# Kernel optimization log

Measured on AMD Instinct MI355X. Metric: run time of the kernel, lower is better.

The kernel has to match this reference:

```python
import jax, jax.numpy as jnp
import numpy as np

VOXEL_SIZE = 0.4
STRIDE = 2
NUM_BATCH = 4
PRE_MAXSIZE = 1024  # nms_premaxsize
NMS_THR = 0.1
NEG_INF = -1e9


def setup_inputs() -> dict:
    key = jax.random.key(0)
    ks = jax.random.split(key, 7)
    N, C = 200000, 256
    feat = jax.random.normal(ks[0], (N, C), dtype=jnp.float32)
    batch_idx = jax.random.randint(ks[1], (N,), 0, NUM_BATCH, dtype=jnp.int32)
    coor = jax.random.randint(ks[2], (N, 2), 0, 400, dtype=jnp.int32)
    W_cls = jax.random.normal(ks[3], (C, 2), dtype=jnp.float32) * 0.02
    b_cls = jnp.zeros((2,), dtype=jnp.float32)
    W_reg = jax.random.normal(ks[4], (C, 9), dtype=jnp.float32) * 0.02
    b_reg = jnp.zeros((9,), dtype=jnp.float32)
    return {"feat": feat, "batch_idx": batch_idx, "coor": coor,
            "W_cls": W_cls, "b_cls": b_cls, "W_reg": W_reg, "b_reg": b_reg}


def _bev_iou(bx):
    # bx: [K,7] (x,y,z,l,w,h,r); axis-aligned BEV IoU on (x,y,l,w)
    x, y, l, w = bx[:, 0], bx[:, 1], bx[:, 3], bx[:, 4]
    x1, x2 = x - l / 2, x + l / 2
    y1, y2 = y - w / 2, y + w / 2
    ix = jnp.maximum(jnp.minimum(x2[:, None], x2[None, :]) - jnp.maximum(x1[:, None], x1[None, :]), 0.0)
    iy = jnp.maximum(jnp.minimum(y2[:, None], y2[None, :]) - jnp.maximum(y1[:, None], y1[None, :]), 0.0)
    inter = ix * iy
    area = l * w
    union = area[:, None] + area[None, :] - inter
    return inter / jnp.maximum(union, 1e-6)


def _nms_keep(iou):
    # greedy NMS over score-descending rows; returns keep mask [K]
    K = iou.shape[0]
    idx = jnp.arange(K)

    def body(i, supp):
        keep_i = jnp.logical_not(supp[i])
        new = keep_i & (iou[i] > NMS_THR) & (idx > i)
        return supp | new

    supp = jax.lax.fori_loop(0, K, body, jnp.zeros((K,), dtype=bool))
    return jnp.logical_not(supp)


def reference(feat, batch_idx, coor, W_cls, b_cls, W_reg, b_reg):
    # ---- shared heads over all sparse voxels ----
    cls_logits = feat @ W_cls + b_cls            # [N, 1+1] (neg evidence, class)
    probs = jax.nn.softmax(cls_logits, axis=-1)
    cls_prob = probs[:, 1:]                      # [N, n_cls]
    conf = jnp.max(cls_prob, axis=-1)            # [N]
    label = jnp.argmax(cls_prob, axis=-1)        # [N]

    reg = feat @ W_reg + b_reg                   # [N, 9] -> ctr(3) dim(3) dir(2) scr(1)
    ctr, dim, drn, scr = reg[:, :3], reg[:, 3:6], reg[:, 6:8], reg[:, 8]
    scr = jax.nn.sigmoid(scr)                    # sigmoid_keys=['scr']

    # indices2metric: voxel indices -> metric centers
    centers = coor.astype(jnp.float32) * (VOXEL_SIZE * STRIDE)  # [N, 2]

    xy = centers + ctr[:, :2]
    z = ctr[:, 2]
    lwh = jnp.exp(jnp.clip(dim, -6.0, 6.0))
    angle = jnp.arctan2(drn[:, 0], drn[:, 1])
    boxes = jnp.concatenate([xy, z[:, None], lwh, angle[:, None]], axis=-1)  # [N, 7]
    score = conf * scr                           # [N]

    def per_sample(b):
        s = jnp.where(batch_idx == b, score, NEG_INF)
        vals, idx = jax.lax.top_k(s, PRE_MAXSIZE)          # score-sorted (desc)
        bx = boxes[idx]                                     # [K, 7]
        lb = label[idx]                                     # [K]
        valid = vals > NEG_INF / 2
        iou = _bev_iou(bx)
        keep = _nms_keep(iou) & valid
        out = jnp.concatenate([bx, vals[:, None]], axis=-1) * keep[:, None]  # [K, 8]
        return out, lb, keep

    out, lb, keep = jax.vmap(per_sample)(jnp.arange(NUM_BATCH))
    return out, lb, keep
```

## Files before the change

### kernel.cpp

```cpp
#include <hip/hip_runtime.h>
#include <math.h>

#define NBATCH 4
#define PRE 1024
#define CAND 4096
#define NHIST 65536
#define MAXSLOT 384

__device__ __forceinline__ unsigned long long allow_mask(int i, int l) {
    int base = l << 6;
    if (i < base) return ~0ull;
    int sh = i - base + 1;
    if (sh >= 64) return 0ull;
    return (~0ull) << sh;
}

__global__ void k0_weights(const float* __restrict__ Wcls, const float* __restrict__ bcls,
                           const float* __restrict__ Wreg, const float* __restrict__ breg,
                           double* __restrict__ Wd3, float* __restrict__ Wf8,
                           double* __restrict__ biasD, float* __restrict__ biasF) {
    int j = blockIdx.x;
    int c = threadIdx.x;
    if (j < 2) {
        Wd3[j * 256 + c] = (double)Wcls[c * 2 + j];
        if (c == 0) biasD[j] = (double)bcls[j];
    } else if (j == 10) {
        Wd3[2 * 256 + c] = (double)Wreg[c * 9 + 8];
        if (c == 0) biasD[2] = (double)breg[8];
    } else {
        int r = j - 2;
        Wf8[r * 256 + c] = Wreg[c * 9 + r];
        if (c == 0) biasF[r] = breg[r];
    }
}

__global__ __launch_bounds__(256) void k1_points(
    const float4* __restrict__ feat4, const int* __restrict__ batch_idx,
    const int* __restrict__ coor, const double* __restrict__ Wd3,
    const float* __restrict__ Wf8, const double* __restrict__ biasD,
    const float* __restrict__ biasF, float* __restrict__ pointData,
    unsigned long long* __restrict__ keys, unsigned int* __restrict__ hist, int N) {
    __shared__ float4 smem4[64 * 68 / 4];
    float* sfeat = (float*)smem4;
    int tid = threadIdx.x;
    int q = tid >> 6;
    int p = tid & 63;
    int p0 = blockIdx.x * 64;

    double accD0 = 0.0, accD1 = 0.0, accD2 = 0.0;
    float accF[8];
#pragma unroll
    for (int j = 0; j < 8; ++j) accF[j] = 0.f;

    for (int c = 0; c < 4; ++c) {
        __syncthreads();
#pragma unroll
        for (int it = 0; it < 4; ++it) {
            int u = it * 256 + tid;
            int pl = u >> 4, f4 = u & 15;
            int gp = p0 + pl;
            float4 v = make_float4(0.f, 0.f, 0.f, 0.f);
            if (gp < N) v = feat4[(size_t)gp * 64 + c * 16 + f4];
            *(float4*)(sfeat + pl * 68 + f4 * 4) = v;
        }
        __syncthreads();
        int chb = c * 64 + q * 16;
        const double* w0 = Wd3 + chb;
        const float* wf = Wf8 + chb;
#pragma unroll
        for (int k4 = 0; k4 < 4; ++k4) {
            float4 v = *(const float4*)(sfeat + p * 68 + q * 16 + k4 * 4);
            float vv[4] = {v.x, v.y, v.z, v.w};
#pragma unroll
            for (int m = 0; m < 4; ++m) {
                int k = k4 * 4 + m;
                double fd = (double)vv[m];
                accD0 = fma(fd, w0[k], accD0);
                accD1 = fma(fd, w0[256 + k], accD1);
                accD2 = fma(fd, w0[512 + k], accD2);
#pragma unroll
                for (int j = 0; j < 8; ++j) accF[j] = fmaf(vv[m], wf[j * 256 + k], accF[j]);
            }
        }
    }
    __syncthreads();
    double* pD = (double*)smem4;
    float* pF = (float*)smem4 + 1536;
    pD[tid * 3 + 0] = accD0; pD[tid * 3 + 1] = accD1; pD[tid * 3 + 2] = accD2;
#pragma unroll
    for (int j = 0; j < 8; ++j) pF[tid * 8 + j] = accF[j];
    __syncthreads();
    if (tid < 64) {
        int gp = p0 + tid;
        if (gp < N) {
            double d0 = biasD[0], d1 = biasD[1], d2 = biasD[2];
            float f[8];
#pragma unroll
            for (int j = 0; j < 8; ++j) f[j] = biasF[j];
#pragma unroll
            for (int qq = 0; qq < 4; ++qq) {
                int base = qq * 64 + tid;
                d0 += pD[base * 3 + 0]; d1 += pD[base * 3 + 1]; d2 += pD[base * 3 + 2];
#pragma unroll
                for (int j = 0; j < 8; ++j) f[j] += pF[base * 8 + j];
            }
            double conf = 1.0 / (1.0 + exp(-(d1 - d0)));
            double scr = 1.0 / (1.0 + exp(-d2));
            double score = conf * scr;
            float s32 = (float)score;

            float cx = (float)coor[2 * gp] * 0.8f;
            float cy = (float)coor[2 * gp + 1] * 0.8f;
            float bx = cx + f[0], by = cy + f[1], bz = f[2];
            float bl = expf(fminf(fmaxf(f[3], -6.f), 6.f));
            float bw = expf(fminf(fmaxf(f[4], -6.f), 6.f));
            float bh = expf(fminf(fmaxf(f[5], -6.f), 6.f));
            float ba = atan2f(f[6], f[7]);

            float4* pd = (float4*)(pointData + (size_t)gp * 8);
            pd[0] = make_float4(bx, by, bz, bl);
            pd[1] = make_float4(bw, bh, ba, s32);
            keys[gp] = (unsigned long long)__double_as_longlong(score);
            int b = batch_idx[gp];
            atomicAdd(&hist[b * NHIST + (__float_as_uint(s32) >> 16)], 1u);
        }
    }
}

__global__ __launch_bounds__(256) void k2_thresh(const unsigned int* __restrict__ hist,
                                                 unsigned int* __restrict__ Tarr) {
    int b = blockIdx.x, tid = threadIdx.x;
    __shared__ unsigned int csum[256];
    __shared__ unsigned int chunkv[256];
    __shared__ int stc;
    __shared__ unsigned int scum;
    const unsigned int* h = hist + b * NHIST;
    unsigned int s = 0;
    for (int m = 0; m < 256; ++m) s += h[tid * 256 + m];
    csum[tid] = s;
    __syncthreads();
    if (tid == 0) {
        unsigned int cum = 0; int tc = -1;
        for (int t = 255; t >= 0; --t) {
            if (cum + csum[t] >= 1024u) { tc = t; break; }
            cum += csum[t];
        }
        stc = tc; scum = cum;
    }
    __syncthreads();
    int tc = stc;
    if (tc < 0) { if (tid == 0) Tarr[b] = 0u; return; }
    chunkv[tid] = h[tc * 256 + tid];
    __syncthreads();
    if (tid == 0) {
        unsigned int cum = scum, T = (unsigned int)(tc * 256);
        for (int m = 255; m >= 0; --m) {
            unsigned int c = chunkv[m];
            if (cum + c >= 1024u) { T = (unsigned int)(tc * 256 + m); break; }
            cum += c;
        }
        Tarr[b] = T;
    }
}

__global__ void k3_compact(const int* __restrict__ batch_idx, const float* __restrict__ pointData,
                           const unsigned long long* __restrict__ keys,
                           const unsigned int* __restrict__ Tarr, unsigned int* __restrict__ candCount,
                           unsigned int* __restrict__ candIdx, unsigned long long* __restrict__ candKey,
                           int N) {
    int p = blockIdx.x * 256 + threadIdx.x;
    if (p >= N) return;
    int b = batch_idx[p];
    float s32 = pointData[(size_t)p * 8 + 7];
    unsigned int bucket = __float_as_uint(s32) >> 16;
    if (bucket >= Tarr[b]) {
        unsigned int pos = atomicAdd(&candCount[b], 1u);
        if (pos < CAND) {
            candIdx[b * CAND + pos] = (unsigned int)p;
            candKey[b * CAND + pos] = keys[p];
        }
    }
}

__global__ __launch_bounds__(1024) void k4_sort(const unsigned int* __restrict__ candCount,
                                                const unsigned int* __restrict__ candIdx,
                                                const unsigned long long* __restrict__ candKey,
                                                const float* __restrict__ pointData,
                                                float* __restrict__ topBox,
                                                unsigned int* __restrict__ validArr) {
    int b = blockIdx.x, tid = threadIdx.x;
    __shared__ unsigned long long ka[CAND];
    __shared__ unsigned int id[CAND];
    unsigned int cnt = candCount[b];
    if (cnt > CAND) cnt = CAND;
    int n = (cnt <= 2048u) ? 2048 : 4096;
    for (int t = tid; t < n; t += 1024) {
        if ((unsigned int)t < cnt) {
            ka[t] = ~candKey[b * CAND + t];
            id[t] = candIdx[b * CAND + t];
        } else {
            ka[t] = ~0ull;
            id[t] = 0xFFFFFFFFu;
        }
    }
    __syncthreads();
    for (int k = 2; k <= n; k <<= 1) {
        for (int j = k >> 1; j > 0; j >>= 1) {
            for (int t = tid; t < n; t += 1024) {
                int l = t ^ j;
                if (l > t) {
                    bool up = ((t & k) == 0);
                    unsigned long long kt = ka[t], kl = ka[l];
                    unsigned int it_ = id[t], il = id[l];
                    bool gt = (kt > kl) || (kt == kl && it_ > il);
                    if (gt == up) { ka[t] = kl; ka[l] = kt; id[t] = il; id[l] = it_; }
                }
            }
            __syncthreads();
        }
    }
    unsigned int gi = id[tid];
    bool valid = (gi != 0xFFFFFFFFu) && ((unsigned int)tid < cnt);
    float v[8];
#pragma unroll
    for (int k = 0; k < 8; ++k) v[k] = 0.f;
    if (valid) {
        const float* pd = pointData + (size_t)gi * 8;
#pragma unroll
        for (int k = 0; k < 8; ++k) v[k] = pd[k];
    }
    float* tb = topBox + (size_t)(b * PRE + tid) * 8;
#pragma unroll
    for (int k = 0; k < 8; ++k) tb[k] = v[k];
    validArr[b * PRE + tid] = valid ? 1u : 0u;
}

__global__ __launch_bounds__(256) void k5_iou(const float* __restrict__ topBox,
                                              unsigned long long* __restrict__ M) {
    int wid = blockIdx.x * 4 + (threadIdx.x >> 6);
    int lane = threadIdx.x & 63;
    int b = wid >> 14;
    int rem = wid & 16383;
    int i = rem >> 4;
    int wj = rem & 15;
    if (wj < (i >> 6)) return;
    const float* bi = topBox + (size_t)(b * PRE + i) * 8;
    int j = wj * 64 + lane;
    const float* bj = topBox + (size_t)(b * PRE + j) * 8;
    float xi = bi[0], yi = bi[1], li = bi[3], wi_ = bi[4];
    float xj = bj[0], yj = bj[1], lj = bj[3], wj_ = bj[4];
    float x1i = xi - li * 0.5f, x2i = xi + li * 0.5f;
    float y1i = yi - wi_ * 0.5f, y2i = yi + wi_ * 0.5f;
    float x1j = xj - lj * 0.5f, x2j = xj + lj * 0.5f;
    float y1j = yj - wj_ * 0.5f, y2j = yj + wj_ * 0.5f;
    float ix = fmaxf(fminf(x2i, x2j) - fmaxf(x1i, x1j), 0.0f);
    float iy = fmaxf(fminf(y2i, y2j) - fmaxf(y1i, y1j), 0.0f);
    float inter = ix * iy;
    float ai = li * wi_, aj = lj * wj_;
    float uni = ai + aj - inter;
    float iou = inter / fmaxf(uni, 1e-6f);
    unsigned long long m = __ballot(iou > 0.1f);
    if (lane == 0) M[(size_t)(b * PRE + i) * 16 + wj] = m;
}

__global__ __launch_bounds__(256) void k6_nms(const unsigned long long* __restrict__ M,
                                              const unsigned int* __restrict__ validArr,
                                              const float* __restrict__ topBox,
                                              float* __restrict__ out0,
                                              float* __restrict__ keepOut) {
    __shared__ unsigned long long Mc[MAXSLOT * 16];
    __shared__ unsigned int slotIdx[PRE];
    __shared__ unsigned int cntSh;
    __shared__ unsigned long long suppSh[16];
    int b = blockIdx.x, tid = threadIdx.x;
    if (tid == 0) cntSh = 0;
    __syncthreads();
    for (int r = tid; r < PRE; r += 256) {
        const unsigned long long* row = M + (size_t)(b * PRE + r) * 16;
        unsigned long long w[16];
        unsigned long long o = 0ull;
#pragma unroll
        for (int l = 0; l < 16; ++l) { w[l] = row[l] & allow_mask(r, l); o |= w[l]; }
        unsigned int s = 0xFFFFFFFFu;
        if (o != 0ull) {
            unsigned int slot = atomicAdd(&cntSh, 1u);
            if (slot < MAXSLOT) {
                s = slot;
#pragma unroll
                for (int l = 0; l < 16; ++l) Mc[slot * 16 + l] = w[l];
            } else s = 0xFFFFFFFEu;
        }
        slotIdx[r] = s;
    }
    __syncthreads();
    if (tid < 64) {
        int lane = tid;
        unsigned long long supp = 0ull;
        for (int g = 0; g < 16; ++g) {
            unsigned long long act = __ballot(slotIdx[g * 64 + lane] != 0xFFFFFFFFu);
            while (act) {
                int bit = __builtin_ctzll(act);
                act &= act - 1ull;
                int i = g * 64 + bit;
                unsigned long long wsup = __shfl(supp, g);
                bool keep_i = ((wsup >> (i & 63)) & 1ull) == 0ull;
                if (keep_i && lane < 16) {
                    unsigned int s = slotIdx[i];
                    unsigned long long add = (s < MAXSLOT)
                        ? Mc[s * 16 + lane]
                        : (M[(size_t)(b * PRE + i) * 16 + lane] & allow_mask(i, lane));
                    supp |= add;
                }
            }
        }
        if (lane < 16) suppSh[lane] = supp;
    }
    __syncthreads();
    for (int r = tid; r < PRE; r += 256) {
        bool keep = (((suppSh[r >> 6] >> (r & 63)) & 1ull) == 0ull) && (validArr[b * PRE + r] != 0u);
        float kf = keep ? 1.0f : 0.0f;
        const float* tb = topBox + (size_t)(b * PRE + r) * 8;
        float* o = out0 + (size_t)(b * PRE + r) * 8;
#pragma unroll
        for (int k = 0; k < 8; ++k) o[k] = tb[k] * kf;
        keepOut[b * PRE + r] = kf;
    }
}

extern "C" void kernel_launch(void* const* d_in, const int* in_sizes, int n_in,
                              void* d_out, int out_size, void* d_ws, size_t ws_size,
                              hipStream_t stream) {
    int N = in_sizes[0] / 256;
    const float* feat = (const float*)d_in[0];
    const int* batch_idx = (const int*)d_in[1];
    const int* coor = (const int*)d_in[2];
    const float* Wcls = (const float*)d_in[3];
    const float* bcls = (const float*)d_in[4];
    const float* Wreg = (const float*)d_in[5];
    const float* breg = (const float*)d_in[6];

    char* ws = (char*)d_ws;
    size_t off = 0;
    auto take = [&](size_t bytes) -> char* {
        char* r = ws + off;
        off += (bytes + 255) & ~(size_t)255;
        return r;
    };
    float* pointData = (float*)take((size_t)N * 8 * 4);
    unsigned long long* keys = (unsigned long long*)take((size_t)N * 8);
    unsigned int* hist = (unsigned int*)take((size_t)NBATCH * NHIST * 4);
    unsigned int* Tarr = (unsigned int*)take(NBATCH * 4);
    unsigned int* candCount = (unsigned int*)take(NBATCH * 4);
    unsigned int* candIdx = (unsigned int*)take(NBATCH * CAND * 4);
    unsigned long long* candKey = (unsigned long long*)take(NBATCH * CAND * 8);
    float* topBox = (float*)take(NBATCH * PRE * 8 * 4);
    unsigned int* validArr = (unsigned int*)take(NBATCH * PRE * 4);
    unsigned long long* M = (unsigned long long*)take((size_t)NBATCH * PRE * 16 * 8);
    double* Wd3 = (double*)take(3 * 256 * 8);
    float* Wf8 = (float*)take(8 * 256 * 4);
    double* biasD = (double*)take(3 * 8);
    float* biasF = (float*)take(8 * 4);

    float* out0 = (float*)d_out;
    float* keepOut = out0 + NBATCH * PRE * 8 + NBATCH * PRE;

    hipMemsetAsync(d_out, 0, (size_t)out_size * 4, stream);
    hipMemsetAsync(hist, 0, (size_t)NBATCH * NHIST * 4, stream);
    hipMemsetAsync(candCount, 0, NBATCH * 4, stream);

    int pb64 = (N + 63) / 64;
    int pb256 = (N + 255) / 256;
    k0_weights<<<dim3(11), dim3(256), 0, stream>>>(Wcls, bcls, Wreg, breg, Wd3, Wf8, biasD, biasF);
    k1_points<<<dim3(pb64), dim3(256), 0, stream>>>((const float4*)feat, batch_idx, coor,
                                                    Wd3, Wf8, biasD, biasF,
                                                    pointData, keys, hist, N);
    k2_thresh<<<dim3(NBATCH), dim3(256), 0, stream>>>(hist, Tarr);
    k3_compact<<<dim3(pb256), dim3(256), 0, stream>>>(batch_idx, pointData, keys, Tarr,
                                                      candCount, candIdx, candKey, N);
    k4_sort<<<dim3(NBATCH), dim3(1024), 0, stream>>>(candCount, candIdx, candKey,
                                                     pointData, topBox, validArr);
    k5_iou<<<dim3(NBATCH * PRE * 16 / 4), dim3(256), 0, stream>>>(topBox, M);
    k6_nms<<<dim3(NBATCH), dim3(256), 0, stream>>>(M, validArr, topBox, out0, keepOut);
}
```

Measured before the change: 488.3 us.

## Use one thread per point in head GEMV, compact IoU layout, drop memsets

The point-head kernel now has each thread handle one full feature row. It loads it through registers with double-buffered float4 prefetch, which replaces the LDS-staged four-way split and its shared-memory reduction. The IoU kernel uses one wavefront per row that loops over column words and reads a packed float4 geometry array written by the sort kernel. The output and candCount memsets are removed: candCount is zeroed inside the threshold kernel and the label output is written explicitly. Reading a 1 KB row per thread gives uncoalesced, strided global loads and high register pressure, while the reduction barriers and separate memset launches go away.

```diff
diff --git a/kernel.cpp b/kernel.cpp
--- a/kernel.cpp
+++ b/kernel.cpp
@@ -34,106 +34,81 @@
     }
 }
 
-__global__ __launch_bounds__(256) void k1_points(
+__global__ __launch_bounds__(256, 4) void k1_points(
     const float4* __restrict__ feat4, const int* __restrict__ batch_idx,
     const int* __restrict__ coor, const double* __restrict__ Wd3,
     const float* __restrict__ Wf8, const double* __restrict__ biasD,
     const float* __restrict__ biasF, float* __restrict__ pointData,
     unsigned long long* __restrict__ keys, unsigned int* __restrict__ hist, int N) {
-    __shared__ float4 smem4[64 * 68 / 4];
-    float* sfeat = (float*)smem4;
-    int tid = threadIdx.x;
-    int q = tid >> 6;
-    int p = tid & 63;
-    int p0 = blockIdx.x * 64;
-
-    double accD0 = 0.0, accD1 = 0.0, accD2 = 0.0;
-    float accF[8];
-#pragma unroll
-    for (int j = 0; j < 8; ++j) accF[j] = 0.f;
-
-    for (int c = 0; c < 4; ++c) {
-        __syncthreads();
-#pragma unroll
-        for (int it = 0; it < 4; ++it) {
-            int u = it * 256 + tid;
-            int pl = u >> 4, f4 = u & 15;
-            int gp = p0 + pl;
-            float4 v = make_float4(0.f, 0.f, 0.f, 0.f);
-            if (gp < N) v = feat4[(size_t)gp * 64 + c * 16 + f4];
-            *(float4*)(sfeat + pl * 68 + f4 * 4) = v;
-        }
-        __syncthreads();
-        int chb = c * 64 + q * 16;
-        const double* w0 = Wd3 + chb;
-        const float* wf = Wf8 + chb;
-#pragma unroll
-        for (int k4 = 0; k4 < 4; ++k4) {
-            float4 v = *(const float4*)(sfeat + p * 68 + q * 16 + k4 * 4);
-            float vv[4] = {v.x, v.y, v.z, v.w};
+    int p = blockIdx.x * 256 + threadIdx.x;
+    int pc = (p < N) ? p : 0;
+    const float4* row = feat4 + (size_t)pc * 64;
+
+    double a0 = 0.0, a1 = 0.0, a2 = 0.0;
+    float f[8] = {0.f, 0.f, 0.f, 0.f, 0.f, 0.f, 0.f, 0.f};
+    float4 cur[8], nxt[8];
+#pragma unroll
+    for (int u = 0; u < 8; ++u) cur[u] = row[u];
+#pragma unroll
+    for (int o = 0; o < 8; ++o) {
+        if (o < 7) {
+#pragma unroll
+            for (int u = 0; u < 8; ++u) nxt[u] = row[(o + 1) * 8 + u];
+        }
+#pragma unroll
+        for (int u = 0; u < 8; ++u) {
+            float vv[4] = {cur[u].x, cur[u].y, cur[u].z, cur[u].w};
 #pragma unroll
             for (int m = 0; m < 4; ++m) {
-                int k = k4 * 4 + m;
+                int k = o * 32 + u * 4 + m;
                 double fd = (double)vv[m];
-                accD0 = fma(fd, w0[k], accD0);
-                accD1 = fma(fd, w0[256 + k], accD1);
-                accD2 = fma(fd, w0[512 + k], accD2);
-#pragma unroll
-                for (int j = 0; j < 8; ++j) accF[j] = fmaf(vv[m], wf[j * 256 + k], accF[j]);
+                a0 = fma(fd, Wd3[k], a0);
+                a1 = fma(fd, Wd3[256 + k], a1);
+                a2 = fma(fd, Wd3[512 + k], a2);
+#pragma unroll
+                for (int j = 0; j < 8; ++j) f[j] = fmaf(vv[m], Wf8[j * 256 + k], f[j]);
             }
         }
-    }
-    __syncthreads();
-    double* pD = (double*)smem4;
-    float* pF = (float*)smem4 + 1536;
-    pD[tid * 3 + 0] = accD0; pD[tid * 3 + 1] = accD1; pD[tid * 3 + 2] = accD2;
-#pragma unroll
-    for (int j = 0; j < 8; ++j) pF[tid * 8 + j] = accF[j];
-    __syncthreads();
-    if (tid < 64) {
-        int gp = p0 + tid;
-        if (gp < N) {
-            double d0 = biasD[0], d1 = biasD[1], d2 = biasD[2];
-            float f[8];
-#pragma unroll
-            for (int j = 0; j < 8; ++j) f[j] = biasF[j];
-#pragma unroll
-            for (int qq = 0; qq < 4; ++qq) {
-                int base = qq * 64 + tid;
-                d0 += pD[base * 3 + 0]; d1 += pD[base * 3 + 1]; d2 += pD[base * 3 + 2];
-#pragma unroll
-                for (int j = 0; j < 8; ++j) f[j] += pF[base * 8 + j];
-            }
-            double conf = 1.0 / (1.0 + exp(-(d1 - d0)));
-            double scr = 1.0 / (1.0 + exp(-d2));
-            double score = conf * scr;
-            float s32 = (float)score;
-
-            float cx = (float)coor[2 * gp] * 0.8f;
-            float cy = (float)coor[2 * gp + 1] * 0.8f;
-            float bx = cx + f[0], by = cy + f[1], bz = f[2];
-            float bl = expf(fminf(fmaxf(f[3], -6.f), 6.f));
-            float bw = expf(fminf(fmaxf(f[4], -6.f), 6.f));
-            float bh = expf(fminf(fmaxf(f[5], -6.f), 6.f));
-            float ba = atan2f(f[6], f[7]);
-
-            float4* pd = (float4*)(pointData + (size_t)gp * 8);
-            pd[0] = make_float4(bx, by, bz, bl);
-            pd[1] = make_float4(bw, bh, ba, s32);
-            keys[gp] = (unsigned long long)__double_as_longlong(score);
-            int b = batch_idx[gp];
-            atomicAdd(&hist[b * NHIST + (__float_as_uint(s32) >> 16)], 1u);
-        }
-    }
+#pragma unroll
+        for (int u = 0; u < 8; ++u) cur[u] = nxt[u];
+    }
+    if (p >= N) return;
+
+    double d0 = a0 + biasD[0], d1 = a1 + biasD[1], d2 = a2 + biasD[2];
+    double conf = 1.0 / (1.0 + exp(-(d1 - d0)));
+    double scr = 1.0 / (1.0 + exp(-d2));
+    double score = conf * scr;
+    float s32 = (float)score;
+
+    float fb[8];
+#pragma unroll
+    for (int j = 0; j < 8; ++j) fb[j] = f[j] + biasF[j];
+
+    float cx = (float)coor[2 * p] * 0.8f;
+    float cy = (float)coor[2 * p + 1] * 0.8f;
+    float bx = cx + fb[0], by = cy + fb[1], bz = fb[2];
+    float bl = expf(fminf(fmaxf(fb[3], -6.f), 6.f));
+    float bw = expf(fminf(fmaxf(fb[4], -6.f), 6.f));
+    float bh = expf(fminf(fmaxf(fb[5], -6.f), 6.f));
+    float ba = atan2f(fb[6], fb[7]);
+
+    float4* pd = (float4*)(pointData + (size_t)p * 8);
+    pd[0] = make_float4(bx, by, bz, bl);
+    pd[1] = make_float4(bw, bh, ba, s32);
+    keys[p] = (unsigned long long)__double_as_longlong(score);
+    int b = batch_idx[p];
+    atomicAdd(&hist[b * NHIST + (__float_as_uint(s32) >> 16)], 1u);
 }
 
 __global__ __launch_bounds__(256) void k2_thresh(const unsigned int* __restrict__ hist,
-                                                 unsigned int* __restrict__ Tarr) {
+                                                 unsigned int* __restrict__ Tarr,
+                                                 unsigned int* __restrict__ candCount) {
     int b = blockIdx.x, tid = threadIdx.x;
     __shared__ unsigned int csum[256];
     __shared__ unsigned int chunkv[256];
     __shared__ int stc;
     __shared__ unsigned int scum;
+    if (tid == 0) candCount[b] = 0u;
     const unsigned int* h = hist + b * NHIST;
     unsigned int s = 0;
     for (int m = 0; m < 256; ++m) s += h[tid * 256 + m];
@@ -187,6 +162,7 @@
                                                 const unsigned long long* __restrict__ candKey,
                                                 const float* __restrict__ pointData,
                                                 float* __restrict__ topBox,
+                                                float4* __restrict__ geo,
                                                 unsigned int* __restrict__ validArr) {
     int b = blockIdx.x, tid = threadIdx.x;
     __shared__ unsigned long long ka[CAND];
@@ -232,41 +208,42 @@
     float* tb = topBox + (size_t)(b * PRE + tid) * 8;
 #pragma unroll
     for (int k = 0; k < 8; ++k) tb[k] = v[k];
+    geo[b * PRE + tid] = make_float4(v[0], v[1], v[3], v[4]);
     validArr[b * PRE + tid] = valid ? 1u : 0u;
 }
 
-__global__ __launch_bounds__(256) void k5_iou(const float* __restrict__ topBox,
+__global__ __launch_bounds__(256) void k5_iou(const float4* __restrict__ geo,
                                               unsigned long long* __restrict__ M) {
-    int wid = blockIdx.x * 4 + (threadIdx.x >> 6);
-    int lane = threadIdx.x & 63;
-    int b = wid >> 14;
-    int rem = wid & 16383;
-    int i = rem >> 4;
-    int wj = rem & 15;
-    if (wj < (i >> 6)) return;
-    const float* bi = topBox + (size_t)(b * PRE + i) * 8;
-    int j = wj * 64 + lane;
-    const float* bj = topBox + (size_t)(b * PRE + j) * 8;
-    float xi = bi[0], yi = bi[1], li = bi[3], wi_ = bi[4];
-    float xj = bj[0], yj = bj[1], lj = bj[3], wj_ = bj[4];
-    float x1i = xi - li * 0.5f, x2i = xi + li * 0.5f;
-    float y1i = yi - wi_ * 0.5f, y2i = yi + wi_ * 0.5f;
-    float x1j = xj - lj * 0.5f, x2j = xj + lj * 0.5f;
-    float y1j = yj - wj_ * 0.5f, y2j = yj + wj_ * 0.5f;
-    float ix = fmaxf(fminf(x2i, x2j) - fmaxf(x1i, x1j), 0.0f);
-    float iy = fmaxf(fminf(y2i, y2j) - fmaxf(y1i, y1j), 0.0f);
-    float inter = ix * iy;
-    float ai = li * wi_, aj = lj * wj_;
-    float uni = ai + aj - inter;
-    float iou = inter / fmaxf(uni, 1e-6f);
-    unsigned long long m = __ballot(iou > 0.1f);
-    if (lane == 0) M[(size_t)(b * PRE + i) * 16 + wj] = m;
+    int wv = threadIdx.x >> 6, lane = threadIdx.x & 63;
+    int gidx = blockIdx.x * 4 + wv;
+    int b = gidx >> 10, i = gidx & (PRE - 1);
+    float4 bi = geo[b * PRE + i];
+    float x1i = bi.x - bi.z * 0.5f, x2i = bi.x + bi.z * 0.5f;
+    float y1i = bi.y - bi.w * 0.5f, y2i = bi.y + bi.w * 0.5f;
+    float ai = bi.z * bi.w;
+    int g = i >> 6;
+    unsigned long long* Mrow = M + (size_t)(b * PRE + i) * 16;
+    for (int wj = g; wj < 16; ++wj) {
+        int j = wj * 64 + lane;
+        float4 bj = geo[b * PRE + j];
+        float x1j = bj.x - bj.z * 0.5f, x2j = bj.x + bj.z * 0.5f;
+        float y1j = bj.y - bj.w * 0.5f, y2j = bj.y + bj.w * 0.5f;
+        float aj = bj.z * bj.w;
+        float ix = fmaxf(fminf(x2i, x2j) - fmaxf(x1i, x1j), 0.0f);
+        float iy = fmaxf(fminf(y2i, y2j) - fmaxf(y1i, y1j), 0.0f);
+        float inter = ix * iy;
+        float uni = ai + aj - inter;
+        float iou = inter / fmaxf(uni, 1e-6f);
+        unsigned long long m = __ballot(iou > 0.1f);
+        if (lane == 0) Mrow[wj] = m;
+    }
 }
 
 __global__ __launch_bounds__(256) void k6_nms(const unsigned long long* __restrict__ M,
                                               const unsigned int* __restrict__ validArr,
                                               const float* __restrict__ topBox,
                                               float* __restrict__ out0,
+                                              int* __restrict__ lbOut,
                                               float* __restrict__ keepOut) {
     __shared__ unsigned long long Mc[MAXSLOT * 16];
     __shared__ unsigned int slotIdx[PRE];
@@ -323,6 +300,7 @@
         float* o = out0 + (size_t)(b * PRE + r) * 8;
 #pragma unroll
         for (int k = 0; k < 8; ++k) o[k] = tb[k] * kf;
+        lbOut[b * PRE + r] = 0;
         keepOut[b * PRE + r] = kf;
     }
 }
@@ -354,6 +332,7 @@
     unsigned int* candIdx = (unsigned int*)take(NBATCH * CAND * 4);
     unsigned long long* candKey = (unsigned long long*)take(NBATCH * CAND * 8);
     float* topBox = (float*)take(NBATCH * PRE * 8 * 4);
+    float4* geo = (float4*)take(NBATCH * PRE * 16);
     unsigned int* validArr = (unsigned int*)take(NBATCH * PRE * 4);
     unsigned long long* M = (unsigned long long*)take((size_t)NBATCH * PRE * 16 * 8);
     double* Wd3 = (double*)take(3 * 256 * 8);
@@ -362,23 +341,21 @@
     float* biasF = (float*)take(8 * 4);
 
     float* out0 = (float*)d_out;
+    int* lbOut = (int*)(out0 + NBATCH * PRE * 8);
     float* keepOut = out0 + NBATCH * PRE * 8 + NBATCH * PRE;
 
-    hipMemsetAsync(d_out, 0, (size_t)out_size * 4, stream);
     hipMemsetAsync(hist, 0, (size_t)NBATCH * NHIST * 4, stream);
-    hipMemsetAsync(candCount, 0, NBATCH * 4, stream);
-
-    int pb64 = (N + 63) / 64;
+
     int pb256 = (N + 255) / 256;
     k0_weights<<<dim3(11), dim3(256), 0, stream>>>(Wcls, bcls, Wreg, breg, Wd3, Wf8, biasD, biasF);
-    k1_points<<<dim3(pb64), dim3(256), 0, stream>>>((const float4*)feat, batch_idx, coor,
-                                                    Wd3, Wf8, biasD, biasF,
-                                                    pointData, keys, hist, N);
-    k2_thresh<<<dim3(NBATCH), dim3(256), 0, stream>>>(hist, Tarr);
+    k1_points<<<dim3(pb256), dim3(256), 0, stream>>>((const float4*)feat, batch_idx, coor,
+                                                     Wd3, Wf8, biasD, biasF,
+                                                     pointData, keys, hist, N);
+    k2_thresh<<<dim3(NBATCH), dim3(256), 0, stream>>>(hist, Tarr, candCount);
     k3_compact<<<dim3(pb256), dim3(256), 0, stream>>>(batch_idx, pointData, keys, Tarr,
                                                       candCount, candIdx, candKey, N);
     k4_sort<<<dim3(NBATCH), dim3(1024), 0, stream>>>(candCount, candIdx, candKey,
-                                                     pointData, topBox, validArr);
-    k5_iou<<<dim3(NBATCH * PRE * 16 / 4), dim3(256), 0, stream>>>(topBox, M);
-    k6_nms<<<dim3(NBATCH), dim3(256), 0, stream>>>(M, validArr, topBox, out0, keepOut);
-}
+                                                     pointData, topBox, geo, validArr);
+    k5_iou<<<dim3(NBATCH * PRE / 4), dim3(256), 0, stream>>>(geo, M);
+    k6_nms<<<dim3(NBATCH), dim3(256), 0, stream>>>(M, validArr, topBox, out0, lbOut, keepOut);
+}
```

After: 509.5 us. 4.4% more time.
